# Kernel tuning notes

Measured on AMD Instinct MI355X. Metric: run time of the kernel, lower is better.

The kernel has to match this reference:

```python
import jax, jax.numpy as jnp
import numpy as np

B, S = 2, 1024
HIDDEN = 2048
NUM_K, NUM_V = 16, 32
DK, DV = 128, 128
KCONV = 4
EPS = 1e-6
KEY_DIM = NUM_K * DK      # 2048
VAL_DIM = NUM_V * DV      # 4096
RATIO = NUM_V // NUM_K    # 2


def setup_inputs() -> dict:
    key = jax.random.key(0)
    ks = jax.random.split(key, 8)
    sc = lambda k, shape, s=0.02: jax.random.normal(k, shape, jnp.float32) * s
    return {
        "hidden_states": jax.random.normal(ks[0], (B, S, HIDDEN), jnp.float32),
        "W_qkvz": sc(ks[1], (HIDDEN, 2 * KEY_DIM + 2 * VAL_DIM)),
        "W_ba": sc(ks[2], (HIDDEN, 2 * NUM_V)),
        "conv_weight": sc(ks[3], (2 * KEY_DIM + VAL_DIM, KCONV), 0.1),
        "A_log": jnp.log(jax.random.uniform(ks[4], (NUM_V,), jnp.float32, 0.001, 16.0)),
        "dt_bias": jnp.ones((NUM_V,), jnp.float32),
        "norm_weight": jnp.ones((DV,), jnp.float32),
        "W_out": sc(ks[5], (VAL_DIM, HIDDEN)),
    }


def _l2norm(x):
    return x * jax.lax.rsqrt(jnp.sum(x * x, axis=-1, keepdims=True) + 1e-6)


def reference(hidden_states, W_qkvz, W_ba, conv_weight, A_log, dt_bias, norm_weight, W_out):
    Bb, Ss, _ = hidden_states.shape
    # fused in_proj + fix_query_key_value_ordering: per k-head layout [q|k|ratio*v|ratio*z]
    qkvz = (hidden_states @ W_qkvz).reshape(Bb, Ss, NUM_K, 2 * DK + 2 * RATIO * DV)
    q = qkvz[..., :DK]                                        # [B,S,NUM_K,DK]
    k = qkvz[..., DK:2 * DK]
    v = qkvz[..., 2 * DK:2 * DK + RATIO * DV].reshape(Bb, Ss, NUM_V, DV)
    z = qkvz[..., 2 * DK + RATIO * DV:].reshape(Bb, Ss, NUM_V, DV)
    ba = (hidden_states @ W_ba).reshape(Bb, Ss, NUM_K, 2 * RATIO)
    b = ba[..., :RATIO].reshape(Bb, Ss, NUM_V)
    a = ba[..., RATIO:].reshape(Bb, Ss, NUM_V)
    # causal depthwise conv over mixed qkv channels + silu (causal_conv1d)
    mixed = jnp.concatenate(
        [q.reshape(Bb, Ss, -1), k.reshape(Bb, Ss, -1), v.reshape(Bb, Ss, -1)], axis=-1)
    x = jnp.transpose(mixed, (0, 2, 1))                       # [B,C,S]
    x = jnp.pad(x, ((0, 0), (0, 0), (KCONV - 1, 0)))
    conv = jax.lax.conv_general_dilated(
        x, conv_weight[:, None, :], (1,), 'VALID',
        feature_group_count=x.shape[1],
        dimension_numbers=('NCH', 'OIH', 'NCH'))
    mixed = jax.nn.silu(jnp.transpose(conv, (0, 2, 1)))       # [B,S,conv_dim]
    q = mixed[..., :KEY_DIM].reshape(Bb, Ss, NUM_K, DK)
    k = mixed[..., KEY_DIM:2 * KEY_DIM].reshape(Bb, Ss, NUM_K, DK)
    v = mixed[..., 2 * KEY_DIM:].reshape(Bb, Ss, NUM_V, DV)
    # GQA: repeat each k-head to its RATIO consecutive v-heads
    q = jnp.repeat(q, RATIO, axis=2)
    k = jnp.repeat(k, RATIO, axis=2)
    q = _l2norm(q) * (DK ** -0.5)
    k = _l2norm(k)
    # fused_gdn_gating: g = -exp(A_log) * softplus(a + dt_bias); beta = sigmoid(b)
    g = -jnp.exp(A_log) * jax.nn.softplus(a + dt_bias)        # [B,S,H] fp32
    beta = jax.nn.sigmoid(b)
    # recurrent gated delta rule scan; state [B,H,DK,DV]
    def step(state, inp):
        qt, kt, vt, gt, bt = inp
        state = state * jnp.exp(gt)[..., None, None]
        pred = jnp.einsum('bhk,bhkv->bhv', kt, state)
        delta = (vt - pred) * bt[..., None]
        state = state + kt[..., None] * delta[..., None, :]
        out = jnp.einsum('bhk,bhkv->bhv', qt, state)
        return state, out

    xs = (q.transpose(1, 0, 2, 3), k.transpose(1, 0, 2, 3), v.transpose(1, 0, 2, 3),
          g.transpose(1, 0, 2), beta.transpose(1, 0, 2))
    state0 = jnp.zeros((Bb, NUM_V, DK, DV), jnp.float32)
    _, core = jax.lax.scan(step, state0, xs)                  # [S,B,H,DV]
    core = core.transpose(1, 0, 2, 3)
    # RMSNormGated (norm_before_gate=True): rmsnorm(x) * w * silu(z)
    var = jnp.mean(core * core, axis=-1, keepdims=True)
    core = core * jax.lax.rsqrt(var + EPS) * norm_weight * jax.nn.silu(z)
    return core.reshape(Bb, Ss, VAL_DIM) @ W_out              # [B,S,HIDDEN]
```

## Files before the change

### kernel.cpp

```cpp
#include <hip/hip_runtime.h>
#include <stdint.h>

#define B_ 2
#define S_ 1024
#define HID 2048
#define NK 16
#define NV 32
#define DK_ 128
#define DV_ 128
#define QKVZ_N 12288
#define TOK (B_*S_)
#define KROW 192

typedef unsigned short u16;
typedef __bf16 bf16x8 __attribute__((ext_vector_type(8)));
typedef float f32x4 __attribute__((ext_vector_type(4)));
typedef float f32x2 __attribute__((ext_vector_type(2)));
typedef unsigned short u16x8 __attribute__((ext_vector_type(8)));
typedef unsigned short u16x4 __attribute__((ext_vector_type(4)));

__device__ __forceinline__ float bf2f(u16 u) {
    return __builtin_bit_cast(float, (unsigned)u << 16);
}
__device__ __forceinline__ u16 f2bf(float f) {
    unsigned u = __builtin_bit_cast(unsigned, f);
    u += 0x7fff + ((u >> 16) & 1);
    return (u16)(u >> 16);
}

template <int CTRL>
__device__ __forceinline__ float dpp_add(float x) {
    int yi = __builtin_amdgcn_update_dpp(0, __builtin_bit_cast(int, x), CTRL, 0xF, 0xF, true);
    return x + __builtin_bit_cast(float, yi);
}
__device__ __forceinline__ float sum16(float x) {
    x = dpp_add<0xB1>(x);
    x = dpp_add<0x4E>(x);
    x = dpp_add<0x141>(x);
    x = dpp_add<0x140>(x);
    return x;
}

__device__ __forceinline__ void gl16(const void* g, void* l) {
    __builtin_amdgcn_global_load_lds((const __attribute__((address_space(1))) uint32_t*)g,
                                     (__attribute__((address_space(3))) uint32_t*)l, 16, 0, 0);
}
__device__ __forceinline__ void gl4(const void* g, void* l) {
    __builtin_amdgcn_global_load_lds((const __attribute__((address_space(1))) uint32_t*)g,
                                     (__attribute__((address_space(3))) uint32_t*)l, 4, 0, 0);
}

__global__ void k_cvt_bf16(const float* __restrict__ in, u16* __restrict__ out, int n) {
    int i = (blockIdx.x * blockDim.x + threadIdx.x) * 4;
    if (i >= n) return;
    float4 v = *(const float4*)(in + i);
    u16x4 o = { f2bf(v.x), f2bf(v.y), f2bf(v.z), f2bf(v.w) };
    *(u16x4*)(out + i) = o;
}

__global__ void k_transpose(const float* __restrict__ in, u16* __restrict__ out, int R, int C) {
    __shared__ float tile[32][33];
    int c0 = blockIdx.x * 32, r0 = blockIdx.y * 32;
    int tx = threadIdx.x, ty = threadIdx.y;
#pragma unroll
    for (int i = 0; i < 4; i++)
        tile[ty + i * 8][tx] = in[(size_t)(r0 + ty + i * 8) * C + c0 + tx];
    __syncthreads();
#pragma unroll
    for (int i = 0; i < 4; i++)
        out[(size_t)(c0 + ty + i * 8) * R + r0 + tx] = f2bf(tile[tx][ty + i * 8]);
}

template <int OUT_BF16>
__global__ __launch_bounds__(256) void k_gemm(const u16* __restrict__ A, const u16* __restrict__ Bt,
                                              void* __restrict__ Cv, int K, int ldc) {
    __shared__ u16 As[128 * 32];
    __shared__ u16 Bs[128 * 32];
    int tid = threadIdx.x;
    int bm = blockIdx.y, bn = blockIdx.x;
    int wid = tid >> 6, lane = tid & 63;
    int wm = wid >> 1, wn = wid & 1;
    int l15 = lane & 15, lg = lane >> 4;
    const u16* src0 = (wid >> 1) ? (Bt + (size_t)bn * 128 * K) : (A + (size_t)bm * 128 * K);
    u16* ldsb = (wid >> 1) ? Bs : As;
    int cbase = (wid & 1) * 4;
    int lrow = lane >> 2, lcol = (lane & 3) * 8;
    f32x4 acc[4][4] = {};
    for (int k0 = 0; k0 < K; k0 += 32) {
        if (k0) __syncthreads();
#pragma unroll
        for (int c = 0; c < 4; c++) {
            int ch = cbase + c;
            gl16(src0 + (size_t)(16 * ch + lrow) * K + k0 + lcol, (char*)ldsb + ch * 1024);
        }
        __syncthreads();
        bf16x8 af[4], bf[4];
#pragma unroll
        for (int mi = 0; mi < 4; mi++)
            af[mi] = __builtin_bit_cast(bf16x8, *(const u16x8*)&As[(wm * 64 + mi * 16 + l15) * 32 + lg * 8]);
#pragma unroll
        for (int ni = 0; ni < 4; ni++)
            bf[ni] = __builtin_bit_cast(bf16x8, *(const u16x8*)&Bs[(wn * 64 + ni * 16 + l15) * 32 + lg * 8]);
#pragma unroll
        for (int mi = 0; mi < 4; mi++)
#pragma unroll
            for (int ni = 0; ni < 4; ni++)
                acc[mi][ni] = __builtin_amdgcn_mfma_f32_16x16x32_bf16(af[mi], bf[ni], acc[mi][ni], 0, 0, 0);
    }
#pragma unroll
    for (int mi = 0; mi < 4; mi++) {
        int gr0 = bm * 128 + wm * 64 + mi * 16 + lg * 4;
#pragma unroll
        for (int ni = 0; ni < 4; ni++) {
            int gc = bn * 128 + wn * 64 + ni * 16 + l15;
#pragma unroll
            for (int r = 0; r < 4; r++) {
                if (OUT_BF16)
                    ((u16*)Cv)[(size_t)(gr0 + r) * ldc + gc] = f2bf(acc[mi][ni][r]);
                else
                    ((float*)Cv)[(size_t)(gr0 + r) * ldc + gc] = acc[mi][ni][r];
            }
        }
    }
}

__global__ void k_ba(const float* __restrict__ hid, const float* __restrict__ Wba, float* __restrict__ ba) {
    int token = blockIdx.x;
    int c = threadIdx.x;
    const float* h = hid + (size_t)token * HID;
    const float* w = Wba + c;
    float acc = 0.f;
    for (int k = 0; k < HID; k += 4) {
        float4 hv = *(const float4*)(h + k);
        acc += hv.x * w[(size_t)k * 64] + hv.y * w[(size_t)(k + 1) * 64] +
               hv.z * w[(size_t)(k + 2) * 64] + hv.w * w[(size_t)(k + 3) * 64];
    }
    ba[(size_t)token * 64 + c] = acc;
}

__global__ __launch_bounds__(256) void k_conv(const u16* __restrict__ qkvz, const float* __restrict__ ba,
                                              const float* __restrict__ cw, const float* __restrict__ A_log,
                                              const float* __restrict__ dt_bias, float* __restrict__ qs,
                                              float* __restrict__ ks, float* __restrict__ vs,
                                              float2* __restrict__ gb2) {
    __shared__ float sm[4096];
    int token = blockIdx.x;
    int b = token >> 10;
    int t = token & (S_ - 1);
    int tid = threadIdx.x;
    const u16* row3 = qkvz + (size_t)token * QKVZ_N;
#pragma unroll
    for (int i = 0; i < 32; i++) {
        int c = tid + i * 256;
        int col;
        if (c < 2048) col = (c >> 7) * 768 + (c & 127);
        else if (c < 4096) col = ((c - 2048) >> 7) * 768 + 128 + (c & 127);
        else {
            int cc = c - 4096;
            col = (cc >> 8) * 768 + 256 + ((cc >> 7) & 1) * 128 + (cc & 127);
        }
        float4 w = *(const float4*)(cw + c * 4);
        float x3 = bf2f(row3[col]);
        float x2 = (t >= 1) ? bf2f(row3[col - QKVZ_N]) : 0.f;
        float x1 = (t >= 2) ? bf2f(row3[col - 2 * QKVZ_N]) : 0.f;
        float x0 = (t >= 3) ? bf2f(row3[col - 3 * QKVZ_N]) : 0.f;
        float s = w.x * x0 + w.y * x1 + w.z * x2 + w.w * x3;
        s = s / (1.f + __expf(-s));
        if (c < 4096) sm[c] = s;
        else {
            int cc = c - 4096;
            int hv = cc >> 7, d = cc & 127;
            vs[((size_t)(b * NV + hv) * S_ + t) * 128 + d] = s;
        }
    }
    __syncthreads();
    int grp = tid >> 3, l8 = tid & 7;
    float vals[16];
    float ss = 0.f;
    const float* sp = sm + grp * 128 + l8 * 16;
#pragma unroll
    for (int i = 0; i < 16; i++) { vals[i] = sp[i]; ss += vals[i] * vals[i]; }
    ss += __shfl_xor(ss, 1); ss += __shfl_xor(ss, 2); ss += __shfl_xor(ss, 4);
    float scale = rsqrtf(ss + 1e-6f);
    if (grp < 16) scale *= 0.08838834764831845f;
    float* op = (grp < 16 ? qs : ks) + ((size_t)(b * NK + (grp & 15)) * S_ + t) * KROW + 24 * l8;
    *(float4*)(op)      = make_float4(vals[0]*scale, vals[1]*scale, vals[2]*scale, vals[3]*scale);
    *(float4*)(op + 4)  = make_float4(vals[4]*scale, vals[5]*scale, vals[6]*scale, vals[7]*scale);
    *(float4*)(op + 12) = make_float4(vals[8]*scale, vals[9]*scale, vals[10]*scale, vals[11]*scale);
    *(float4*)(op + 16) = make_float4(vals[12]*scale, vals[13]*scale, vals[14]*scale, vals[15]*scale);
    if (tid < 32) {
        int hv = tid;
        float bval = ba[(size_t)token * 64 + (hv >> 1) * 4 + (hv & 1)];
        float aval = ba[(size_t)token * 64 + (hv >> 1) * 4 + 2 + (hv & 1)];
        float x = aval + dt_bias[hv];
        float sp2 = (x > 20.f) ? x : log1pf(__expf(x));
        float eg = __expf(-__expf(A_log[hv]) * sp2);
        float bt = 1.f / (1.f + __expf(-bval));
        gb2[(size_t)(b * NV + hv) * S_ + t] = make_float2(eg, bt);
    }
}

__global__ __launch_bounds__(512) void k_scan(const float* __restrict__ qs, const float* __restrict__ ks,
                                              const float* __restrict__ vs, const float2* __restrict__ gb2,
                                              float* __restrict__ core) {
    __shared__ float kb[2][32 * KROW];
    __shared__ float qb[2][32 * KROW];
    __shared__ float vbf[2][32 * 32];
    __shared__ float2 gbl[2][32];
    __shared__ float outb[2][32 * 32];
    int bid = blockIdx.x;
    int bh = bid >> 2, vsp = bid & 3;
    int b = bh >> 5, hv = bh & 31, hk = hv >> 1;
    int tid = threadIdx.x;
    int wid = tid >> 6, lane = tid & 63;
    int vloc = tid >> 4, rq = tid & 15;
    const char* kgb = (const char*)(ks + (size_t)(b * NK + hk) * S_ * KROW);
    const char* qgb = (const char*)(qs + (size_t)(b * NK + hk) * S_ * KROW);
    const char* vgb = (const char*)(vs + ((size_t)(b * NV + hv) * S_) * 128 + vsp * 32);
    const char* ggb = (const char*)(gb2 + (size_t)(b * NV + hv) * S_);
    float* cpb = core + ((size_t)(b * NV + hv) * S_) * 128 + vsp * 32;
    bool writer = (rq == 0);
    int koff = 12 * rq;

    auto stage = [&](int tile, int bufi) {
        const char* kg = kgb + (size_t)tile * (32 * KROW * 4);
        const char* qg = qgb + (size_t)tile * (32 * KROW * 4);
        const char* vg = vgb + (size_t)tile * 32 * 512;
        const char* gg = ggb + (size_t)tile * 256;
        for (int ch = wid; ch < 53; ch += 8) {
            if (ch < 24)
                gl16(kg + ch * 1024 + lane * 16, (char*)&kb[bufi][0] + ch * 1024);
            else if (ch < 48)
                gl16(qg + (ch - 24) * 1024 + lane * 16, (char*)&qb[bufi][0] + (ch - 24) * 1024);
            else if (ch < 52) {
                int c4 = ch - 48;
                gl16(vg + (size_t)(c4 * 8 + (lane >> 3)) * 512 + (lane & 7) * 16,
                     (char*)&vbf[bufi][0] + c4 * 1024);
            } else
                gl4(gg + lane * 4, (char*)&gbl[bufi][0]);
        }
    };

    f32x2 st2[4] = {};
    stage(0, 0);
    __syncthreads();
    for (int tile = 0; tile < 32; ++tile) {
        int buf = tile & 1;
        if (tile < 31) stage(tile + 1, buf ^ 1);
        const float* kT = &kb[buf][0];
        const float* qT = &qb[buf][0];
        const float* vT = &vbf[buf][0];
        const float2* gT = &gbl[buf][0];
        float* oT = &outb[buf][0];
#pragma unroll
        for (int t = 0; t < 32; ++t) {
            f32x4 kA = *(const f32x4*)(kT + t * KROW + koff);
            f32x4 kB = *(const f32x4*)(kT + t * KROW + koff + 4);
            f32x4 qA = *(const f32x4*)(qT + t * KROW + koff);
            f32x4 qB = *(const f32x4*)(qT + t * KROW + koff + 4);
            float vv = vT[t * 32 + vloc];
            float2 gv = gT[t];
            f32x2 k0 = __builtin_shufflevector(kA, kA, 0, 1);
            f32x2 k1 = __builtin_shufflevector(kA, kA, 2, 3);
            f32x2 k2 = __builtin_shufflevector(kB, kB, 0, 1);
            f32x2 k3 = __builtin_shufflevector(kB, kB, 2, 3);
            f32x2 pa = __builtin_elementwise_fma(k1, st2[1], k0 * st2[0]);
            f32x2 pb = __builtin_elementwise_fma(k3, st2[3], k2 * st2[2]);
            float dks = sum16((pa.x + pb.x) + (pa.y + pb.y));
            float eg = gv.x;
            float delta = (vv - eg * dks) * gv.y;
            f32x2 e2 = {eg, eg}, d2 = {delta, delta};
            st2[0] = __builtin_elementwise_fma(st2[0], e2, k0 * d2);
            st2[1] = __builtin_elementwise_fma(st2[1], e2, k1 * d2);
            st2[2] = __builtin_elementwise_fma(st2[2], e2, k2 * d2);
            st2[3] = __builtin_elementwise_fma(st2[3], e2, k3 * d2);
            f32x2 q0 = __builtin_shufflevector(qA, qA, 0, 1);
            f32x2 q1 = __builtin_shufflevector(qA, qA, 2, 3);
            f32x2 q2 = __builtin_shufflevector(qB, qB, 0, 1);
            f32x2 q3 = __builtin_shufflevector(qB, qB, 2, 3);
            f32x2 oa = __builtin_elementwise_fma(q1, st2[1], q0 * st2[0]);
            f32x2 ob = __builtin_elementwise_fma(q3, st2[3], q2 * st2[2]);
            float dqs = sum16((oa.x + ob.x) + (oa.y + ob.y));
            if (writer) oT[t * 32 + vloc] = dqs;
        }
        __syncthreads();
        {
            int trow = tid >> 4, c2 = (tid & 15) * 2;
            f32x2 val = *(const f32x2*)&outb[buf][trow * 32 + c2];
            *(f32x2*)(cpb + (size_t)(tile * 32 + trow) * 128 + c2) = val;
        }
    }
}

__global__ __launch_bounds__(256) void k_gate(const float* __restrict__ core, const u16* __restrict__ qkvz,
                                              const float* __restrict__ nw, u16* __restrict__ gated) {
    int token = blockIdx.x, tid = threadIdx.x;
    int b = token >> 10, t = token & (S_ - 1);
    int grp = tid >> 3, l8 = tid & 7;
    const float* cp = core + ((size_t)(b * NV + grp) * S_ + t) * DV_ + l8 * 16;
    float vals[16];
    float ss = 0.f;
#pragma unroll
    for (int i = 0; i < 16; i++) { vals[i] = cp[i]; ss += vals[i] * vals[i]; }
    ss += __shfl_xor(ss, 1); ss += __shfl_xor(ss, 2); ss += __shfl_xor(ss, 4);
    float rms = rsqrtf(ss * (1.0f / DV_) + 1e-6f);
    const u16* zp = qkvz + (size_t)token * QKVZ_N + (grp >> 1) * 768 + 512 + (grp & 1) * 128 + l8 * 16;
    u16* op = gated + ((size_t)token * NV + grp) * DV_ + l8 * 16;
#pragma unroll
    for (int i = 0; i < 16; i++) {
        float z = bf2f(zp[i]);
        float sz = z / (1.f + __expf(-z));
        op[i] = f2bf(vals[i] * rms * nw[l8 * 16 + i] * sz);
    }
}

extern "C" void kernel_launch(void* const* d_in, const int* in_sizes, int n_in,
                              void* d_out, int out_size, void* d_ws, size_t ws_size,
                              hipStream_t stream) {
    const float* hidden = (const float*)d_in[0];
    const float* Wqkvz = (const float*)d_in[1];
    const float* Wba = (const float*)d_in[2];
    const float* convw = (const float*)d_in[3];
    const float* A_log = (const float*)d_in[4];
    const float* dt_bias = (const float*)d_in[5];
    const float* norm_w = (const float*)d_in[6];
    const float* Wout = (const float*)d_in[7];

    char* ws = (char*)d_ws;
    size_t off = 0;
    auto alloc = [&](size_t bytes) -> void* {
        void* p = ws + off;
        off += (bytes + 255) & ~(size_t)255;
        return p;
    };
    u16* hiddenB = (u16*)alloc((size_t)TOK * HID * 2);
    u16* WqT = (u16*)alloc((size_t)QKVZ_N * HID * 2);
    u16* WoT = (u16*)alloc((size_t)HID * 4096 * 2);
    u16* qkvz = (u16*)alloc((size_t)TOK * QKVZ_N * 2);
    float* ba = (float*)alloc((size_t)TOK * 64 * 4);
    float* qs = (float*)alloc((size_t)B_ * NK * S_ * KROW * 4);
    float* ks = (float*)alloc((size_t)B_ * NK * S_ * KROW * 4);
    float* vs = (float*)alloc((size_t)B_ * NV * S_ * 128 * 4);
    float2* gb2 = (float2*)alloc((size_t)B_ * NV * S_ * 8);
    float* core = (float*)alloc((size_t)B_ * NV * S_ * 128 * 4);
    u16* gated = (u16*)alloc((size_t)TOK * 4096 * 2);

    k_cvt_bf16<<<4096, 256, 0, stream>>>(hidden, hiddenB, TOK * HID);
    k_transpose<<<dim3(QKVZ_N / 32, HID / 32), dim3(32, 8), 0, stream>>>(Wqkvz, WqT, HID, QKVZ_N);
    k_transpose<<<dim3(HID / 32, 4096 / 32), dim3(32, 8), 0, stream>>>(Wout, WoT, 4096, HID);
    k_gemm<1><<<dim3(QKVZ_N / 128, TOK / 128), 256, 0, stream>>>(hiddenB, WqT, qkvz, HID, QKVZ_N);
    k_ba<<<TOK, 64, 0, stream>>>(hidden, Wba, ba);
    k_conv<<<TOK, 256, 0, stream>>>(qkvz, ba, convw, A_log, dt_bias, qs, ks, vs, gb2);
    k_scan<<<256, 512, 0, stream>>>(qs, ks, vs, gb2, core);
    k_gate<<<TOK, 256, 0, stream>>>(core, qkvz, norm_w, gated);
    k_gemm<0><<<dim3(HID / 128, TOK / 128), 256, 0, stream>>>(gated, WoT, d_out, 4096, HID);
}
```

Baseline: 612.5 us.

## Replace sequential delta-rule scan with chunked WY-form using MFMA

Replaces the token-by-token recurrent scan with a chunked (64-token) gated delta rule. A prep kernel builds the intra-chunk decayed QK and KK matrices with MFMA. A solve kernel performs the triangular inversion. A chunk kernel carries state across chunks through bf16 hi/lo split MFMA matmuls. Q, K and V are now stored as bf16 instead of fp32, which cuts memory traffic and turns the serial per-step work into matrix-core work, at the cost of extra intermediate buffers, bf16 precision risk in the inputs, and a serial 16-chunk loop over only 128 blocks.

```diff
diff --git a/kernel.cpp b/kernel.cpp
--- a/kernel.cpp
+++ b/kernel.cpp
@@ -10,12 +10,10 @@
 #define DV_ 128
 #define QKVZ_N 12288
 #define TOK (B_*S_)
-#define KROW 192
 
 typedef unsigned short u16;
 typedef __bf16 bf16x8 __attribute__((ext_vector_type(8)));
 typedef float f32x4 __attribute__((ext_vector_type(4)));
-typedef float f32x2 __attribute__((ext_vector_type(2)));
 typedef unsigned short u16x8 __attribute__((ext_vector_type(8)));
 typedef unsigned short u16x4 __attribute__((ext_vector_type(4)));
 
@@ -28,26 +26,17 @@
     return (u16)(u >> 16);
 }
 
-template <int CTRL>
-__device__ __forceinline__ float dpp_add(float x) {
-    int yi = __builtin_amdgcn_update_dpp(0, __builtin_bit_cast(int, x), CTRL, 0xF, 0xF, true);
-    return x + __builtin_bit_cast(float, yi);
-}
-__device__ __forceinline__ float sum16(float x) {
-    x = dpp_add<0xB1>(x);
-    x = dpp_add<0x4E>(x);
-    x = dpp_add<0x141>(x);
-    x = dpp_add<0x140>(x);
-    return x;
-}
-
 __device__ __forceinline__ void gl16(const void* g, void* l) {
     __builtin_amdgcn_global_load_lds((const __attribute__((address_space(1))) uint32_t*)g,
                                      (__attribute__((address_space(3))) uint32_t*)l, 16, 0, 0);
 }
-__device__ __forceinline__ void gl4(const void* g, void* l) {
-    __builtin_amdgcn_global_load_lds((const __attribute__((address_space(1))) uint32_t*)g,
-                                     (__attribute__((address_space(3))) uint32_t*)l, 4, 0, 0);
+
+__device__ __forceinline__ bf16x8 fragld(const u16* base, int row, int col, int rowhw) {
+    int idx = row * rowhw + ((((col >> 3) ^ (row & 7))) << 3);
+    return __builtin_bit_cast(bf16x8, *(const u16x8*)(base + idx));
+}
+__device__ __forceinline__ int swzidx(int row, int col, int rowhw) {
+    return row * rowhw + (((col >> 3) ^ (row & 7)) << 3) + (col & 7);
 }
 
 __global__ void k_cvt_bf16(const float* __restrict__ in, u16* __restrict__ out, int n) {
@@ -140,8 +129,8 @@
 
 __global__ __launch_bounds__(256) void k_conv(const u16* __restrict__ qkvz, const float* __restrict__ ba,
                                               const float* __restrict__ cw, const float* __restrict__ A_log,
-                                              const float* __restrict__ dt_bias, float* __restrict__ qs,
-                                              float* __restrict__ ks, float* __restrict__ vs,
+                                              const float* __restrict__ dt_bias, u16* __restrict__ qsb,
+                                              u16* __restrict__ ksb, u16* __restrict__ vsb,
                                               float2* __restrict__ gb2) {
     __shared__ float sm[4096];
     int token = blockIdx.x;
@@ -170,7 +159,7 @@
         else {
             int cc = c - 4096;
             int hv = cc >> 7, d = cc & 127;
-            vs[((size_t)(b * NV + hv) * S_ + t) * 128 + d] = s;
+            vsb[((size_t)(b * NV + hv) * S_ + t) * 128 + d] = f2bf(s);
         }
     }
     __syncthreads();
@@ -183,112 +172,355 @@
     ss += __shfl_xor(ss, 1); ss += __shfl_xor(ss, 2); ss += __shfl_xor(ss, 4);
     float scale = rsqrtf(ss + 1e-6f);
     if (grp < 16) scale *= 0.08838834764831845f;
-    float* op = (grp < 16 ? qs : ks) + ((size_t)(b * NK + (grp & 15)) * S_ + t) * KROW + 24 * l8;
-    *(float4*)(op)      = make_float4(vals[0]*scale, vals[1]*scale, vals[2]*scale, vals[3]*scale);
-    *(float4*)(op + 4)  = make_float4(vals[4]*scale, vals[5]*scale, vals[6]*scale, vals[7]*scale);
-    *(float4*)(op + 12) = make_float4(vals[8]*scale, vals[9]*scale, vals[10]*scale, vals[11]*scale);
-    *(float4*)(op + 16) = make_float4(vals[12]*scale, vals[13]*scale, vals[14]*scale, vals[15]*scale);
+    u16* op = (grp < 16 ? qsb : ksb) + ((size_t)(b * NK + (grp & 15)) * S_ + t) * 128 + l8 * 16;
+    u16x8 o0, o1;
+#pragma unroll
+    for (int i = 0; i < 8; i++) { o0[i] = f2bf(vals[i] * scale); o1[i] = f2bf(vals[i + 8] * scale); }
+    *(u16x8*)(op) = o0;
+    *(u16x8*)(op + 8) = o1;
     if (tid < 32) {
         int hv = tid;
         float bval = ba[(size_t)token * 64 + (hv >> 1) * 4 + (hv & 1)];
         float aval = ba[(size_t)token * 64 + (hv >> 1) * 4 + 2 + (hv & 1)];
         float x = aval + dt_bias[hv];
         float sp2 = (x > 20.f) ? x : log1pf(__expf(x));
-        float eg = __expf(-__expf(A_log[hv]) * sp2);
+        float graw = -__expf(A_log[hv]) * sp2;
         float bt = 1.f / (1.f + __expf(-bval));
-        gb2[(size_t)(b * NV + hv) * S_ + t] = make_float2(eg, bt);
-    }
-}
-
-__global__ __launch_bounds__(512) void k_scan(const float* __restrict__ qs, const float* __restrict__ ks,
-                                              const float* __restrict__ vs, const float2* __restrict__ gb2,
-                                              float* __restrict__ core) {
-    __shared__ float kb[2][32 * KROW];
-    __shared__ float qb[2][32 * KROW];
-    __shared__ float vbf[2][32 * 32];
-    __shared__ float2 gbl[2][32];
-    __shared__ float outb[2][32 * 32];
+        gb2[(size_t)(b * NV + hv) * S_ + t] = make_float2(graw, bt);
+    }
+}
+
+
+__global__ __launch_bounds__(256) void k_prep(const u16* __restrict__ ksb, const u16* __restrict__ qsb,
+                                              const float2* __restrict__ gb2, float* __restrict__ Mbuf,
+                                              u16* __restrict__ MqB, u16* __restrict__ KtB,
+                                              u16* __restrict__ aQB, float* __restrict__ aCB) {
+    __shared__ u16 Kl[64 * 128];
+    __shared__ u16 Ql[64 * 128];
+    __shared__ float QKKK[64 * 68];
+    __shared__ float cum[64], bet[64], aex[64], gl[64];
     int bid = blockIdx.x;
-    int bh = bid >> 2, vsp = bid & 3;
-    int b = bh >> 5, hv = bh & 31, hk = hv >> 1;
-    int tid = threadIdx.x;
-    int wid = tid >> 6, lane = tid & 63;
-    int vloc = tid >> 4, rq = tid & 15;
-    const char* kgb = (const char*)(ks + (size_t)(b * NK + hk) * S_ * KROW);
-    const char* qgb = (const char*)(qs + (size_t)(b * NK + hk) * S_ * KROW);
-    const char* vgb = (const char*)(vs + ((size_t)(b * NV + hv) * S_) * 128 + vsp * 32);
-    const char* ggb = (const char*)(gb2 + (size_t)(b * NV + hv) * S_);
-    float* cpb = core + ((size_t)(b * NV + hv) * S_) * 128 + vsp * 32;
-    bool writer = (rq == 0);
-    int koff = 12 * rq;
-
-    auto stage = [&](int tile, int bufi) {
-        const char* kg = kgb + (size_t)tile * (32 * KROW * 4);
-        const char* qg = qgb + (size_t)tile * (32 * KROW * 4);
-        const char* vg = vgb + (size_t)tile * 32 * 512;
-        const char* gg = ggb + (size_t)tile * 256;
-        for (int ch = wid; ch < 53; ch += 8) {
-            if (ch < 24)
-                gl16(kg + ch * 1024 + lane * 16, (char*)&kb[bufi][0] + ch * 1024);
-            else if (ch < 48)
-                gl16(qg + (ch - 24) * 1024 + lane * 16, (char*)&qb[bufi][0] + (ch - 24) * 1024);
-            else if (ch < 52) {
-                int c4 = ch - 48;
-                gl16(vg + (size_t)(c4 * 8 + (lane >> 3)) * 512 + (lane & 7) * 16,
-                     (char*)&vbf[bufi][0] + c4 * 1024);
-            } else
-                gl4(gg + lane * 4, (char*)&gbl[bufi][0]);
-        }
-    };
-
-    f32x2 st2[4] = {};
-    stage(0, 0);
-    __syncthreads();
-    for (int tile = 0; tile < 32; ++tile) {
-        int buf = tile & 1;
-        if (tile < 31) stage(tile + 1, buf ^ 1);
-        const float* kT = &kb[buf][0];
-        const float* qT = &qb[buf][0];
-        const float* vT = &vbf[buf][0];
-        const float2* gT = &gbl[buf][0];
-        float* oT = &outb[buf][0];
-#pragma unroll
-        for (int t = 0; t < 32; ++t) {
-            f32x4 kA = *(const f32x4*)(kT + t * KROW + koff);
-            f32x4 kB = *(const f32x4*)(kT + t * KROW + koff + 4);
-            f32x4 qA = *(const f32x4*)(qT + t * KROW + koff);
-            f32x4 qB = *(const f32x4*)(qT + t * KROW + koff + 4);
-            float vv = vT[t * 32 + vloc];
-            float2 gv = gT[t];
-            f32x2 k0 = __builtin_shufflevector(kA, kA, 0, 1);
-            f32x2 k1 = __builtin_shufflevector(kA, kA, 2, 3);
-            f32x2 k2 = __builtin_shufflevector(kB, kB, 0, 1);
-            f32x2 k3 = __builtin_shufflevector(kB, kB, 2, 3);
-            f32x2 pa = __builtin_elementwise_fma(k1, st2[1], k0 * st2[0]);
-            f32x2 pb = __builtin_elementwise_fma(k3, st2[3], k2 * st2[2]);
-            float dks = sum16((pa.x + pb.x) + (pa.y + pb.y));
-            float eg = gv.x;
-            float delta = (vv - eg * dks) * gv.y;
-            f32x2 e2 = {eg, eg}, d2 = {delta, delta};
-            st2[0] = __builtin_elementwise_fma(st2[0], e2, k0 * d2);
-            st2[1] = __builtin_elementwise_fma(st2[1], e2, k1 * d2);
-            st2[2] = __builtin_elementwise_fma(st2[2], e2, k2 * d2);
-            st2[3] = __builtin_elementwise_fma(st2[3], e2, k3 * d2);
-            f32x2 q0 = __builtin_shufflevector(qA, qA, 0, 1);
-            f32x2 q1 = __builtin_shufflevector(qA, qA, 2, 3);
-            f32x2 q2 = __builtin_shufflevector(qB, qB, 0, 1);
-            f32x2 q3 = __builtin_shufflevector(qB, qB, 2, 3);
-            f32x2 oa = __builtin_elementwise_fma(q1, st2[1], q0 * st2[0]);
-            f32x2 ob = __builtin_elementwise_fma(q3, st2[3], q2 * st2[2]);
-            float dqs = sum16((oa.x + ob.x) + (oa.y + ob.y));
-            if (writer) oT[t * 32 + vloc] = dqs;
+    int chunk = bid & 15, hv = (bid >> 4) & 31, b = bid >> 9;
+    int hk = hv >> 1;
+    size_t ch = bid;
+    int tid = threadIdx.x, wid = tid >> 6, lane = tid & 63;
+    int l15 = lane & 15, lg = lane >> 4;
+    const u16* kg = ksb + ((size_t)(b * NK + hk) * S_ + chunk * 64) * 128;
+    const u16* qg = qsb + ((size_t)(b * NK + hk) * S_ + chunk * 64) * 128;
+    for (int c = wid; c < 32; c += 4) {
+        const u16* src = (c < 16) ? kg : qg;
+        u16* dst = (c < 16) ? Kl : Ql;
+        int c1 = c & 15;
+        int row = c1 * 4 + (lane >> 4);
+        int g = lane & 15;
+        gl16(src + row * 128 + ((g ^ (row & 7)) << 3), (char*)dst + c1 * 1024 + lane * 16);
+    }
+    if (tid < 64) {
+        float2 gv = gb2[(size_t)(b * NV + hv) * S_ + chunk * 64 + tid];
+        gl[tid] = gv.x; bet[tid] = gv.y;
+    }
+    __syncthreads();
+    if (tid == 0) { float s = 0.f; for (int i = 0; i < 64; i++) { s += gl[i]; cum[i] = s; } }
+    __syncthreads();
+    if (tid < 64) aex[tid] = __expf(cum[tid]);
+    {
+        f32x4 qk[4] = {};
+#pragma unroll
+        for (int kk = 0; kk < 4; kk++) {
+            bf16x8 af = fragld(Ql, wid * 16 + l15, kk * 32 + lg * 8, 128);
+#pragma unroll
+            for (int nt = 0; nt < 4; nt++) {
+                bf16x8 bk = fragld(Kl, nt * 16 + l15, kk * 32 + lg * 8, 128);
+                qk[nt] = __builtin_amdgcn_mfma_f32_16x16x32_bf16(af, bk, qk[nt], 0, 0, 0);
+            }
+        }
+#pragma unroll
+        for (int nt = 0; nt < 4; nt++)
+#pragma unroll
+            for (int r = 0; r < 4; r++)
+                QKKK[(wid * 16 + lg * 4 + r) * 68 + nt * 16 + l15] = qk[nt][r];
+    }
+    __syncthreads();
+    {
+        int i = tid >> 2, jc = (tid & 3) * 16;
+        u16x8 m0, m1;
+#pragma unroll
+        for (int jj = 0; jj < 16; jj++) {
+            int j = jc + jj;
+            float v = (j <= i) ? __expf(cum[i] - cum[j]) * QKKK[i * 68 + j] : 0.f;
+            if (jj < 8) m0[jj] = f2bf(v); else m1[jj - 8] = f2bf(v);
+        }
+        *(u16x8*)(MqB + ch * 4096 + i * 64 + jc) = m0;
+        *(u16x8*)(MqB + ch * 4096 + i * 64 + jc + 8) = m1;
+    }
+    __syncthreads();
+    {
+        f32x4 kkc[4] = {};
+#pragma unroll
+        for (int kk = 0; kk < 4; kk++) {
+            bf16x8 af = fragld(Kl, wid * 16 + l15, kk * 32 + lg * 8, 128);
+#pragma unroll
+            for (int nt = 0; nt < 4; nt++) {
+                bf16x8 bk = fragld(Kl, nt * 16 + l15, kk * 32 + lg * 8, 128);
+                kkc[nt] = __builtin_amdgcn_mfma_f32_16x16x32_bf16(af, bk, kkc[nt], 0, 0, 0);
+            }
         }
         __syncthreads();
-        {
-            int trow = tid >> 4, c2 = (tid & 15) * 2;
-            f32x2 val = *(const f32x2*)&outb[buf][trow * 32 + c2];
-            *(f32x2*)(cpb + (size_t)(tile * 32 + trow) * 128 + c2) = val;
-        }
+#pragma unroll
+        for (int nt = 0; nt < 4; nt++)
+#pragma unroll
+            for (int r = 0; r < 4; r++)
+                QKKK[(wid * 16 + lg * 4 + r) * 68 + nt * 16 + l15] = kkc[nt][r];
+    }
+    __syncthreads();
+    {
+        int i = tid >> 2, jc = (tid & 3) * 16;
+        float4 out4;
+#pragma unroll
+        for (int q4 = 0; q4 < 4; q4++) {
+#pragma unroll
+            for (int e = 0; e < 4; e++) {
+                int j = jc + q4 * 4 + e;
+                float v = (j < i) ? bet[i] * __expf(cum[i] - cum[j]) * QKKK[i * 68 + j] : 0.f;
+                ((float*)&out4)[e] = v;
+            }
+            *(float4*)(Mbuf + ch * 4096 + i * 64 + jc + q4 * 4) = out4;
+        }
+    }
+    {
+        int dk = tid >> 1, jc = (tid & 1) * 32;
+#pragma unroll
+        for (int q8 = 0; q8 < 4; q8++) {
+            u16x8 o;
+#pragma unroll
+            for (int e = 0; e < 8; e++) {
+                int j = jc + q8 * 8 + e;
+                o[e] = f2bf(__expf(cum[63] - cum[j]) * bf2f(Kl[swzidx(j, dk, 128)]));
+            }
+            *(u16x8*)(KtB + ch * 8192 + dk * 64 + jc + q8 * 8) = o;
+        }
+    }
+    {
+        int i = tid >> 2, dc = (tid & 3) * 32;
+        float a = aex[i];
+#pragma unroll
+        for (int q8 = 0; q8 < 4; q8++) {
+            u16x8 o;
+#pragma unroll
+            for (int e = 0; e < 8; e++)
+                o[e] = f2bf(a * bf2f(Ql[swzidx(i, dc + q8 * 8 + e, 128)]));
+            *(u16x8*)(aQB + ch * 8192 + i * 128 + dc + q8 * 8) = o;
+        }
+    }
+    if (tid == 0) aCB[ch] = aex[63];
+}
+
+__global__ __launch_bounds__(256) void k_solve(const u16* __restrict__ ksb, const u16* __restrict__ vsb,
+                                               const float2* __restrict__ gb2, const float* __restrict__ Mbuf,
+                                               float* __restrict__ TvB, u16* __restrict__ WB) {
+    __shared__ float Ml[64 * 64];
+    __shared__ u16 Kl[64 * 128];
+    __shared__ u16 Vl[64 * 128];
+    __shared__ u16 bounce[64 * 136];
+    __shared__ float cum[64], bet[64], aex[64], gl[64];
+    int bid = blockIdx.x;
+    int chunk = bid & 15, hv = (bid >> 4) & 31, b = bid >> 9;
+    int hk = hv >> 1;
+    size_t ch = bid;
+    int tid = threadIdx.x, wid = tid >> 6, lane = tid & 63;
+    const u16* kg = ksb + ((size_t)(b * NK + hk) * S_ + chunk * 64) * 128;
+    const u16* vg = vsb + ((size_t)(b * NV + hv) * S_ + chunk * 64) * 128;
+    const float* mg = Mbuf + ch * 4096;
+    for (int c = wid; c < 48; c += 4) {
+        if (c < 16) gl16((const char*)mg + c * 1024 + lane * 16, (char*)Ml + c * 1024 + lane * 16);
+        else if (c < 32) gl16((const char*)kg + (c - 16) * 1024 + lane * 16, (char*)Kl + (c - 16) * 1024 + lane * 16);
+        else gl16((const char*)vg + (c - 32) * 1024 + lane * 16, (char*)Vl + (c - 32) * 1024 + lane * 16);
+    }
+    if (tid < 64) {
+        float2 gv = gb2[(size_t)(b * NV + hv) * S_ + chunk * 64 + tid];
+        gl[tid] = gv.x; bet[tid] = gv.y;
+    }
+    __syncthreads();
+    if (tid == 0) { float s = 0.f; for (int i = 0; i < 64; i++) { s += gl[i]; cum[i] = s; } }
+    __syncthreads();
+    if (tid < 64) aex[tid] = __expf(cum[tid]);
+    __syncthreads();
+    int c = tid;
+    float X[64];
+    if (c < 128) {
+#pragma unroll
+        for (int i = 0; i < 64; i++) X[i] = bet[i] * bf2f(Vl[i * 128 + c]);
+    } else {
+        int d = c - 128;
+#pragma unroll
+        for (int i = 0; i < 64; i++) X[i] = -bet[i] * aex[i] * bf2f(Kl[i * 128 + d]);
+    }
+#pragma unroll
+    for (int IB = 0; IB < 8; ++IB) {
+#pragma unroll
+        for (int JB = 0; JB < IB; ++JB) {
+#pragma unroll
+            for (int ii = 0; ii < 8; ++ii) {
+                const float* mr = &Ml[(IB * 8 + ii) * 64 + JB * 8];
+                float4 a = *(const float4*)mr, bq = *(const float4*)(mr + 4);
+                float x = X[IB * 8 + ii];
+                x = fmaf(-a.x, X[JB * 8 + 0], x); x = fmaf(-a.y, X[JB * 8 + 1], x);
+                x = fmaf(-a.z, X[JB * 8 + 2], x); x = fmaf(-a.w, X[JB * 8 + 3], x);
+                x = fmaf(-bq.x, X[JB * 8 + 4], x); x = fmaf(-bq.y, X[JB * 8 + 5], x);
+                x = fmaf(-bq.z, X[JB * 8 + 6], x); x = fmaf(-bq.w, X[JB * 8 + 7], x);
+                X[IB * 8 + ii] = x;
+            }
+        }
+#pragma unroll
+        for (int ii = 1; ii < 8; ++ii) {
+            float x = X[IB * 8 + ii];
+#pragma unroll
+            for (int jj = 0; jj < ii; ++jj)
+                x = fmaf(-Ml[(IB * 8 + ii) * 64 + IB * 8 + jj], X[IB * 8 + jj], x);
+            X[IB * 8 + ii] = x;
+        }
+    }
+    if (c < 128) {
+        float* o = TvB + ch * 8192 + (size_t)c * 64;
+#pragma unroll
+        for (int q4 = 0; q4 < 16; q4++) {
+            float4 v4 = { X[q4 * 4], X[q4 * 4 + 1], X[q4 * 4 + 2], X[q4 * 4 + 3] };
+            *(float4*)(o + q4 * 4) = v4;
+        }
+    } else {
+        int d = c - 128;
+#pragma unroll
+        for (int i = 0; i < 64; i++) bounce[i * 136 + d] = f2bf(X[i]);
+    }
+    __syncthreads();
+    {
+        int i = tid >> 2, dc = (tid & 3) * 32;
+#pragma unroll
+        for (int q8 = 0; q8 < 4; q8++) {
+            u16x8 o;
+#pragma unroll
+            for (int e = 0; e < 8; e++) o[e] = bounce[i * 136 + dc + q8 * 8 + e];
+            *(u16x8*)(WB + ch * 8192 + i * 128 + dc + q8 * 8) = o;
+        }
+    }
+}
+
+__global__ __launch_bounds__(256) void k_chunk(const float* __restrict__ TvB, const u16* __restrict__ WB,
+                                               const u16* __restrict__ aQB, const u16* __restrict__ MqB,
+                                               const u16* __restrict__ KtB, const float* __restrict__ aCB,
+                                               float* __restrict__ core) {
+    __shared__ u16 S0h[64 * 128], S0l[64 * 128];
+    __shared__ u16 DTh[64 * 64], DTl[64 * 64];
+    __shared__ float Tvl[64 * 64];
+    __shared__ u16 Wl[64 * 128], aQl[64 * 128];
+    __shared__ u16 Mql[64 * 64];
+    __shared__ u16 Ktl[128 * 64];
+    int bid = blockIdx.x;
+    int split = bid & 1, bh = bid >> 1;
+    int tid = threadIdx.x, wid = tid >> 6, lane = tid & 63;
+    int l15 = lane & 15, lg = lane >> 4;
+    float4 z4 = {0.f, 0.f, 0.f, 0.f};
+    for (int i = tid; i < 64 * 128 / 8; i += 256) {
+        *(float4*)(S0h + i * 8) = z4;
+        *(float4*)(S0l + i * 8) = z4;
+    }
+    for (int chunk = 0; chunk < 16; ++chunk) {
+        size_t ch = (size_t)bh * 16 + chunk;
+        const char* tvg = (const char*)(TvB + ch * 8192 + (size_t)split * 64 * 64);
+        const char* wg = (const char*)(WB + ch * 8192);
+        const char* qg = (const char*)(aQB + ch * 8192);
+        const char* mg = (const char*)(MqB + ch * 4096);
+        const char* kg = (const char*)(KtB + ch * 8192);
+        for (int c = wid; c < 72; c += 4) {
+            if (c < 16) {
+                gl16(tvg + c * 1024 + lane * 16, (char*)Tvl + c * 1024 + lane * 16);
+            } else if (c < 32) {
+                int cc = c - 16; int row = cc * 4 + (lane >> 4); int g = lane & 15;
+                gl16(wg + row * 256 + ((g ^ (row & 7)) << 4), (char*)Wl + cc * 1024 + lane * 16);
+            } else if (c < 48) {
+                int cc = c - 32; int row = cc * 4 + (lane >> 4); int g = lane & 15;
+                gl16(qg + row * 256 + ((g ^ (row & 7)) << 4), (char*)aQl + cc * 1024 + lane * 16);
+            } else if (c < 56) {
+                int cc = c - 48; int row = cc * 8 + (lane >> 3); int g = lane & 7;
+                gl16(mg + row * 128 + ((g ^ (row & 7)) << 4), (char*)Mql + cc * 1024 + lane * 16);
+            } else {
+                int cc = c - 56; int row = cc * 8 + (lane >> 3); int g = lane & 7;
+                gl16(kg + row * 128 + ((g ^ (row & 7)) << 4), (char*)Ktl + cc * 1024 + lane * 16);
+            }
+        }
+        float aC = aCB[ch];
+        __syncthreads();
+        f32x4 Dacc[4], Oacc[4] = {};
+#pragma unroll
+        for (int nt = 0; nt < 4; nt++)
+#pragma unroll
+            for (int r = 0; r < 4; r++)
+                Dacc[nt][r] = Tvl[(wid * 16 + lg * 4 + r) * 64 + nt * 16 + l15];
+#pragma unroll
+        for (int kk = 0; kk < 4; kk++) {
+            bf16x8 aH = fragld(S0h, wid * 16 + l15, kk * 32 + lg * 8, 128);
+            bf16x8 aL = fragld(S0l, wid * 16 + l15, kk * 32 + lg * 8, 128);
+#pragma unroll
+            for (int nt = 0; nt < 4; nt++) {
+                bf16x8 bW = fragld(Wl, nt * 16 + l15, kk * 32 + lg * 8, 128);
+                Dacc[nt] = __builtin_amdgcn_mfma_f32_16x16x32_bf16(aH, bW,
+                           __builtin_amdgcn_mfma_f32_16x16x32_bf16(aL, bW, Dacc[nt], 0, 0, 0), 0, 0, 0);
+                bf16x8 bQ = fragld(aQl, nt * 16 + l15, kk * 32 + lg * 8, 128);
+                Oacc[nt] = __builtin_amdgcn_mfma_f32_16x16x32_bf16(aH, bQ,
+                           __builtin_amdgcn_mfma_f32_16x16x32_bf16(aL, bQ, Oacc[nt], 0, 0, 0), 0, 0, 0);
+            }
+        }
+#pragma unroll
+        for (int nt = 0; nt < 4; nt++)
+#pragma unroll
+            for (int r = 0; r < 4; r++) {
+                int dv = wid * 16 + lg * 4 + r, t = nt * 16 + l15;
+                float x = Dacc[nt][r];
+                u16 h = f2bf(x);
+                int idx = swzidx(dv, t, 64);
+                DTh[idx] = h; DTl[idx] = f2bf(x - bf2f(h));
+            }
+#pragma unroll
+        for (int kk2 = 0; kk2 < 2; kk2++) {
+            bf16x8 aDh = fragld(DTh, wid * 16 + l15, kk2 * 32 + lg * 8, 64);
+            bf16x8 aDl = fragld(DTl, wid * 16 + l15, kk2 * 32 + lg * 8, 64);
+#pragma unroll
+            for (int nt = 0; nt < 4; nt++) {
+                bf16x8 bM = fragld(Mql, nt * 16 + l15, kk2 * 32 + lg * 8, 64);
+                Oacc[nt] = __builtin_amdgcn_mfma_f32_16x16x32_bf16(aDh, bM,
+                           __builtin_amdgcn_mfma_f32_16x16x32_bf16(aDl, bM, Oacc[nt], 0, 0, 0), 0, 0, 0);
+            }
+        }
+#pragma unroll
+        for (int nt = 0; nt < 4; nt++) {
+            float4 o = { Oacc[nt][0], Oacc[nt][1], Oacc[nt][2], Oacc[nt][3] };
+            size_t t = (size_t)chunk * 64 + nt * 16 + l15;
+            *(float4*)(core + ((size_t)bh * S_ + t) * 128 + split * 64 + wid * 16 + lg * 4) = o;
+        }
+        f32x4 Sacc[8] = {};
+#pragma unroll
+        for (int kk2 = 0; kk2 < 2; kk2++) {
+            bf16x8 aDh = fragld(DTh, wid * 16 + l15, kk2 * 32 + lg * 8, 64);
+            bf16x8 aDl = fragld(DTl, wid * 16 + l15, kk2 * 32 + lg * 8, 64);
+#pragma unroll
+            for (int nd = 0; nd < 8; nd++) {
+                bf16x8 bK = fragld(Ktl, nd * 16 + l15, kk2 * 32 + lg * 8, 64);
+                Sacc[nd] = __builtin_amdgcn_mfma_f32_16x16x32_bf16(aDh, bK,
+                           __builtin_amdgcn_mfma_f32_16x16x32_bf16(aDl, bK, Sacc[nd], 0, 0, 0), 0, 0, 0);
+            }
+        }
+#pragma unroll
+        for (int nd = 0; nd < 8; nd++)
+#pragma unroll
+            for (int r = 0; r < 4; r++) {
+                int dv = wid * 16 + lg * 4 + r, dk = nd * 16 + l15;
+                int idx = swzidx(dv, dk, 128);
+                float old = bf2f(S0h[idx]) + bf2f(S0l[idx]);
+                float nu = fmaf(aC, old, Sacc[nd][r]);
+                u16 h = f2bf(nu);
+                S0h[idx] = h; S0l[idx] = f2bf(nu - bf2f(h));
+            }
+        __syncthreads();
     }
 }
 
@@ -338,10 +570,17 @@
     u16* WoT = (u16*)alloc((size_t)HID * 4096 * 2);
     u16* qkvz = (u16*)alloc((size_t)TOK * QKVZ_N * 2);
     float* ba = (float*)alloc((size_t)TOK * 64 * 4);
-    float* qs = (float*)alloc((size_t)B_ * NK * S_ * KROW * 4);
-    float* ks = (float*)alloc((size_t)B_ * NK * S_ * KROW * 4);
-    float* vs = (float*)alloc((size_t)B_ * NV * S_ * 128 * 4);
+    u16* qsb = (u16*)alloc((size_t)B_ * NK * S_ * 128 * 2);
+    u16* ksb = (u16*)alloc((size_t)B_ * NK * S_ * 128 * 2);
+    u16* vsb = (u16*)alloc((size_t)B_ * NV * S_ * 128 * 2);
     float2* gb2 = (float2*)alloc((size_t)B_ * NV * S_ * 8);
+    float* Mbuf = (float*)alloc((size_t)1024 * 4096 * 4);
+    u16* MqB = (u16*)alloc((size_t)1024 * 4096 * 2);
+    u16* KtB = (u16*)alloc((size_t)1024 * 8192 * 2);
+    u16* aQB = (u16*)alloc((size_t)1024 * 8192 * 2);
+    float* TvB = (float*)alloc((size_t)1024 * 8192 * 4);
+    u16* WB = (u16*)alloc((size_t)1024 * 8192 * 2);
+    float* aCB = (float*)alloc((size_t)1024 * 4);
     float* core = (float*)alloc((size_t)B_ * NV * S_ * 128 * 4);
     u16* gated = (u16*)alloc((size_t)TOK * 4096 * 2);
 
@@ -350,8 +589,10 @@
     k_transpose<<<dim3(HID / 32, 4096 / 32), dim3(32, 8), 0, stream>>>(Wout, WoT, 4096, HID);
     k_gemm<1><<<dim3(QKVZ_N / 128, TOK / 128), 256, 0, stream>>>(hiddenB, WqT, qkvz, HID, QKVZ_N);
     k_ba<<<TOK, 64, 0, stream>>>(hidden, Wba, ba);
-    k_conv<<<TOK, 256, 0, stream>>>(qkvz, ba, convw, A_log, dt_bias, qs, ks, vs, gb2);
-    k_scan<<<256, 512, 0, stream>>>(qs, ks, vs, gb2, core);
+    k_conv<<<TOK, 256, 0, stream>>>(qkvz, ba, convw, A_log, dt_bias, qsb, ksb, vsb, gb2);
+    k_prep<<<1024, 256, 0, stream>>>(ksb, qsb, gb2, Mbuf, MqB, KtB, aQB, aCB);
+    k_solve<<<1024, 256, 0, stream>>>(ksb, vsb, gb2, Mbuf, TvB, WB);
+    k_chunk<<<128, 256, 0, stream>>>(TvB, WB, aQB, MqB, KtB, aCB, core);
     k_gate<<<TOK, 256, 0, stream>>>(core, qkvz, norm_w, gated);
     k_gemm<0><<<dim3(HID / 128, TOK / 128), 256, 0, stream>>>(gated, WoT, d_out, 4096, HID);
 }
```

New measurement: 572.4 us. 1.07x faster.
